# Performance work log

Measured on AMD Instinct MI355X. Metric: run time of the kernel, lower is better.

Reference implementation:

```python
import jax, jax.numpy as jnp
import numpy as np

B, L, D = 4096, 200, 64
N_ITEMS, N_USERS, N_RATINGS = 100000, 100000, 5


def setup_inputs() -> dict:
    key = jax.random.key(0)
    ks = jax.random.split(key, 10)
    nodes = jax.random.randint(ks[0], (B,), 0, N_USERS)
    history_uv = jax.random.randint(ks[1], (B, L), 0, N_ITEMS)
    history_r = jax.random.randint(ks[2], (B, L), 0, N_RATINGS)
    s = 1.0 / np.sqrt(D)
    v2e = jax.random.normal(ks[3], (N_ITEMS, D), dtype=jnp.float32)
    r2e = jax.random.normal(ks[4], (N_RATINGS, D), dtype=jnp.float32)
    # torch Linear: weight is [out, in]
    w1_W = jax.random.uniform(ks[5], (D, 2 * D), dtype=jnp.float32, minval=-s, maxval=s)
    w1_b = jax.random.uniform(ks[6], (D,), dtype=jnp.float32, minval=-s, maxval=s)
    w2_W = jax.random.uniform(ks[7], (D, D), dtype=jnp.float32, minval=-s, maxval=s)
    w2_b = jax.random.uniform(ks[8], (D,), dtype=jnp.float32, minval=-s, maxval=s)
    return {
        "v2e": v2e, "r2e": r2e,
        "w1_W": w1_W, "w1_b": w1_b, "w2_W": w2_W, "w2_b": w2_b,
        "nodes": nodes, "history_uv": history_uv, "history_r": history_r,
    }


def reference(v2e, r2e, w1_W, w1_b, w2_W, w2_b, nodes, history_uv, history_r):
    # Gather item and rating embeddings for every (node, history slot): [B, L, D]
    e_uv = v2e[history_uv]
    e_r = r2e[history_r]
    # concat -> [B, L, 2D], two-layer MLP with ReLU
    x = jnp.concatenate([e_uv, e_r], axis=-1)
    h = jax.nn.relu(jnp.einsum("bli,oi->blo", x, w1_W) + w1_b)
    o = jax.nn.relu(jnp.einsum("bli,oi->blo", h, w2_W) + w2_b)
    # uv=True branch: plain mean over the history dimension (nodes/u2e unused)
    return jnp.mean(o, axis=1)  # [B, D]
```

## Files before the change

kernel.cpp:

```cpp
#include <hip/hip_runtime.h>

#define NITEMS 100000
#define NRATE  5
#define BB     4096
#define LL     200
#define DD     64
#define NBUV   391

typedef short short8  __attribute__((ext_vector_type(8)));
typedef float f32x4   __attribute__((ext_vector_type(4)));
typedef float f32x2   __attribute__((ext_vector_type(2)));
typedef int   i32x4   __attribute__((ext_vector_type(4)));
typedef int   i32x2   __attribute__((ext_vector_type(2)));

static __device__ __forceinline__ short f2bf(float f) {
  return (short)((__builtin_bit_cast(unsigned, f) + 0x8000u) >> 16);
}
static __device__ __forceinline__ unsigned pk2bf(float a, float b) {
  const unsigned ua = __builtin_bit_cast(unsigned, a) + 0x8000u;
  const unsigned ub = __builtin_bit_cast(unsigned, b) + 0x8000u;
  return __builtin_amdgcn_perm(ub, ua, 0x07060302u);
}
static __device__ __forceinline__ int kperm(int p) {
  return ((p & 3) << 4) | (p >> 2);
}

__global__ __launch_bounds__(256) void k_pre(
    const float* __restrict__ v2e, const float* __restrict__ r2e,
    const float* __restrict__ w1W, const float* __restrict__ w1b,
    const float* __restrict__ w2W,
    short* __restrict__ pre_uv, short* __restrict__ w2p,
    float* __restrict__ r5p)
{
  const int tid = threadIdx.x;
  const int blk = blockIdx.x;

  if (blk >= NBUV) {
    for (int idx = tid; idx < 64 * 64; idx += 256) {
      const int o = idx >> 6, p = idx & 63;
      w2p[idx] = f2bf(w2W[o * 64 + kperm(p)]);
    }
    for (int idx = tid; idx < NRATE * 64; idx += 256) {
      const int r = idx >> 6, p = idx & 63;
      const int o = kperm(p);
      const float4* wr = reinterpret_cast<const float4*>(w1W + o * 128 + 64);
      const float4* rr = reinterpret_cast<const float4*>(r2e + r * 64);
      float s = w1b[o];
#pragma unroll
      for (int q = 0; q < 16; ++q) {
        const float4 a = wr[q], b = rr[q];
        s += a.x * b.x + a.y * b.y + a.z * b.z + a.w * b.w;
      }
      r5p[r * 64 + p] = s;
    }
    return;
  }

  const int wave = tid >> 6, lane = tid & 63;
  const int n = lane & 15, quad = lane >> 4;

  short8 bfr[2][4];
#pragma unroll
  for (int nt = 0; nt < 4; ++nt)
#pragma unroll
    for (int kh = 0; kh < 2; ++kh) {
      const float4* p = reinterpret_cast<const float4*>(
          w1W + (nt * 16 + n) * 128 + kh * 32 + quad * 8);
      const float4 x0 = p[0], x1 = p[1];
      i32x4 pk = {(int)pk2bf(x0.x, x0.y), (int)pk2bf(x0.z, x0.w),
                  (int)pk2bf(x1.x, x1.y), (int)pk2bf(x1.z, x1.w)};
      bfr[kh][nt] = __builtin_bit_cast(short8, pk);
    }

  const int ibase_w = blk * 256 + wave * 64;

  float4 cur0, cur1, cur2, cur3;
  {
    const int row = min(ibase_w + n, NITEMS - 1);
    const float4* p = reinterpret_cast<const float4*>(v2e + (size_t)row * 64 + quad * 8);
    cur0 = p[0]; cur1 = p[1];
    const float4* q = reinterpret_cast<const float4*>(v2e + (size_t)row * 64 + 32 + quad * 8);
    cur2 = q[0]; cur3 = q[1];
  }

#pragma unroll
  for (int it = 0; it < 4; ++it) {
    float4 nx0, nx1, nx2, nx3;
    if (it < 3) {
      const int row = min(ibase_w + (it + 1) * 16 + n, NITEMS - 1);
      const float4* p = reinterpret_cast<const float4*>(v2e + (size_t)row * 64 + quad * 8);
      nx0 = p[0]; nx1 = p[1];
      const float4* q = reinterpret_cast<const float4*>(v2e + (size_t)row * 64 + 32 + quad * 8);
      nx2 = q[0]; nx3 = q[1];
    }

    short8 afr[2];
    {
      i32x4 pk0 = {(int)pk2bf(cur0.x, cur0.y), (int)pk2bf(cur0.z, cur0.w),
                   (int)pk2bf(cur1.x, cur1.y), (int)pk2bf(cur1.z, cur1.w)};
      afr[0] = __builtin_bit_cast(short8, pk0);
      i32x4 pk1 = {(int)pk2bf(cur2.x, cur2.y), (int)pk2bf(cur2.z, cur2.w),
                   (int)pk2bf(cur3.x, cur3.y), (int)pk2bf(cur3.z, cur3.w)};
      afr[1] = __builtin_bit_cast(short8, pk1);
    }

    f32x4 d[4];
#pragma unroll
    for (int nt = 0; nt < 4; ++nt) {
      f32x4 z = {0.f, 0.f, 0.f, 0.f};
      z = __builtin_amdgcn_mfma_f32_16x16x32_bf16(afr[0], bfr[0][nt], z, 0, 0, 0);
      z = __builtin_amdgcn_mfma_f32_16x16x32_bf16(afr[1], bfr[1][nt], z, 0, 0, 0);
      d[nt] = z;
    }

#pragma unroll
    for (int r = 0; r < 4; ++r) {
      const int item = ibase_w + it * 16 + quad * 4 + r;
      if (item < NITEMS) {
        i32x2 s = {(int)pk2bf(d[0][r], d[1][r]), (int)pk2bf(d[2][r], d[3][r])};
        *reinterpret_cast<i32x2*>(pre_uv + (size_t)item * 64 + n * 4) = s;
      }
    }

    if (it < 3) { cur0 = nx0; cur1 = nx1; cur2 = nx2; cur3 = nx3; }
  }
}

__global__ __launch_bounds__(256) void k_main(
    const short* __restrict__ pre_uv, const float* __restrict__ r5p,
    const short* __restrict__ w2p, const float* __restrict__ w2b,
    const int* __restrict__ huv, const int* __restrict__ hrr,
    float* __restrict__ out)
{
  __shared__ __align__(16) float s_r5[5 * 68];

  const int tid  = threadIdx.x;
  const int wave = tid >> 6, lane = tid & 63;
  const int n = lane & 15, quad = lane >> 4;
  const int b = blockIdx.x * 4 + wave;

  for (int idx = tid; idx < 5 * 64; idx += 256)
    s_r5[(idx >> 6) * 68 + (idx & 63)] = r5p[idx];

  const int* hu = huv + b * LL;
  const int* hr = hrr + b * LL;

  int iv[13], ir[13];
#pragma unroll
  for (int t = 0; t < 12; ++t) {
    iv[t] = hu[t * 16 + n];
    ir[t] = hr[t * 16 + n];
  }
  {
    const int lc = min(192 + n, LL - 1);
    iv[12] = hu[lc];
    ir[12] = hr[lc];
  }

  short8 u[13][2];
#pragma unroll
  for (int t = 0; t < 13; ++t)
#pragma unroll
    for (int kh = 0; kh < 2; ++kh)
      u[t][kh] = *reinterpret_cast<const short8*>(
          pre_uv + (size_t)iv[t] * 64 + kh * 32 + quad * 8);

  short8 bfr[2][4];
#pragma unroll
  for (int nt = 0; nt < 4; ++nt)
#pragma unroll
    for (int kh = 0; kh < 2; ++kh)
      bfr[kh][nt] = *reinterpret_cast<const short8*>(
          w2p + (nt * 16 + n) * 64 + kh * 32 + quad * 8);

  f32x2 bias2[4];
#pragma unroll
  for (int nt = 0; nt < 4; ++nt) {
    const float bv = w2b[nt * 16 + n];
    bias2[nt] = f32x2{bv, bv};
  }

  __syncthreads();

  const float tailm = (quad < 2) ? 1.0f : 0.0f;
  f32x2 acc2[4] = {{0.f, 0.f}, {0.f, 0.f}, {0.f, 0.f}, {0.f, 0.f}};

#pragma unroll
  for (int t = 0; t < 13; ++t) {
    short8 afr[2];
#pragma unroll
    for (int kh = 0; kh < 2; ++kh) {
      const i32x4 up = __builtin_bit_cast(i32x4, u[t][kh]);
      const f32x2* rp = reinterpret_cast<const f32x2*>(
          s_r5 + ir[t] * 68 + kh * 32 + quad * 8);
      i32x4 hpk;
#pragma unroll
      for (int j = 0; j < 4; ++j) {
        const unsigned p = (unsigned)up[j];
        f32x2 uf = {__builtin_bit_cast(float, p << 16),
                    __builtin_bit_cast(float, p & 0xffff0000u)};
        const f32x2 s = uf + rp[j];
        hpk[j] = (int)pk2bf(fmaxf(s.x, 0.f), fmaxf(s.y, 0.f));
      }
      afr[kh] = __builtin_bit_cast(short8, hpk);
    }

    f32x4 d[4];
#pragma unroll
    for (int nt = 0; nt < 4; ++nt) {
      f32x4 z = {0.f, 0.f, 0.f, 0.f};
      z = __builtin_amdgcn_mfma_f32_16x16x32_bf16(afr[0], bfr[0][nt], z, 0, 0, 0);
      z = __builtin_amdgcn_mfma_f32_16x16x32_bf16(afr[1], bfr[1][nt], z, 0, 0, 0);
      d[nt] = z;
    }

#pragma unroll
    for (int nt = 0; nt < 4; ++nt) {
      f32x2 p0 = f32x2{d[nt][0], d[nt][1]} + bias2[nt];
      f32x2 p1 = f32x2{d[nt][2], d[nt][3]} + bias2[nt];
      p0.x = fmaxf(p0.x, 0.f); p0.y = fmaxf(p0.y, 0.f);
      p1.x = fmaxf(p1.x, 0.f); p1.y = fmaxf(p1.y, 0.f);
      f32x2 s = p0 + p1;
      if (t == 12) { s.x *= tailm; s.y *= tailm; }
      acc2[nt] += s;
    }
  }

  float acc[4];
#pragma unroll
  for (int nt = 0; nt < 4; ++nt) {
    float v = acc2[nt].x + acc2[nt].y;
    v += __shfl_xor(v, 16, 64);
    v += __shfl_xor(v, 32, 64);
    acc[nt] = v;
  }

  out[b * 64 + quad * 16 + n] = acc[quad] * (1.0f / (float)LL);
}

__global__ __launch_bounds__(256) void k_fallback(
    const float* __restrict__ v2e, const float* __restrict__ r2e,
    const float* __restrict__ w1W, const float* __restrict__ w1b,
    const float* __restrict__ w2W, const float* __restrict__ w2b,
    const int* __restrict__ huv, const int* __restrict__ hrr,
    float* __restrict__ out)
{
  __shared__ float sw1[64][129];
  __shared__ float sw2[64][65];
  __shared__ float sx[4][128];
  __shared__ float sh[4][64];
  __shared__ float red[4][64];

  const int tid = threadIdx.x;
  const int wave = tid >> 6, lane = tid & 63;
  const int b = blockIdx.x;

  for (int idx = tid; idx < 64 * 128; idx += 256) sw1[idx >> 7][idx & 127] = w1W[idx];
  for (int idx = tid; idx < 64 * 64; idx += 256) sw2[idx >> 6][idx & 63] = w2W[idx];
  __syncthreads();

  const float b1o = w1b[lane], b2o = w2b[lane];
  float acc = 0.f;

  for (int l = wave; l < LL; l += 4) {
    const int iv = huv[b * LL + l];
    const int ir = hrr[b * LL + l];
    sx[wave][lane]      = v2e[iv * 64 + lane];
    sx[wave][64 + lane] = r2e[ir * 64 + lane];
    __syncthreads();
    float h = b1o;
    for (int i = 0; i < 128; ++i) h += sx[wave][i] * sw1[lane][i];
    sh[wave][lane] = fmaxf(h, 0.f);
    __syncthreads();
    float o = b2o;
    for (int i = 0; i < 64; ++i) o += sh[wave][i] * sw2[lane][i];
    acc += fmaxf(o, 0.f);
  }

  red[wave][lane] = acc;
  __syncthreads();
  if (tid < 64) {
    const float s = red[0][tid] + red[1][tid] + red[2][tid] + red[3][tid];
    out[b * 64 + tid] = s * (1.0f / (float)LL);
  }
}

extern "C" void kernel_launch(void* const* d_in, const int* in_sizes, int n_in,
                              void* d_out, int out_size, void* d_ws, size_t ws_size,
                              hipStream_t stream) {
  (void)in_sizes; (void)n_in; (void)out_size;
  const float* v2e = (const float*)d_in[0];
  const float* r2e = (const float*)d_in[1];
  const float* w1W = (const float*)d_in[2];
  const float* w1b = (const float*)d_in[3];
  const float* w2W = (const float*)d_in[4];
  const float* w2b = (const float*)d_in[5];
  const int* huv = (const int*)d_in[7];
  const int* hrr = (const int*)d_in[8];
  float* out = (float*)d_out;

  const size_t OFF_R5 = (size_t)NITEMS * 64 * sizeof(short);
  const size_t OFF_W2 = OFF_R5 + NRATE * 64 * sizeof(float);
  const size_t NEED   = OFF_W2 + 64 * 64 * sizeof(short);

  if (ws_size >= NEED) {
    short* pre_uv = (short*)d_ws;
    float* r5p    = (float*)((char*)d_ws + OFF_R5);
    short* w2p    = (short*)((char*)d_ws + OFF_W2);

    k_pre<<<NBUV + 1, 256, 0, stream>>>(v2e, r2e, w1W, w1b, w2W, pre_uv, w2p, r5p);
    k_main<<<BB / 4, 256, 0, stream>>>(pre_uv, r5p, w2p, w2b, huv, hrr, out);
  } else {
    k_fallback<<<BB, 256, 0, stream>>>(v2e, r2e, w1W, w1b, w2W, w2b, huv, hrr, out);
  }
}
```

Measured before the change: 115.7 us.

## Grid-stride item tiles in k_pre, per-wave rating table and bias-in-MFMA in k_main

k_pre now launches 512 work blocks, 2048 waves in all, and each wave walks 16-row item tiles with a grid stride of 2048 tiles. The split gives 4 or 3 tiles per wave and drops the bounds clamps, which spreads the v2e projection more evenly over the CUs. k_main gives each wave its own copy of the rating table in LDS, filled by that wave alone, so the block-wide __syncthreads can be removed. It also seeds the MFMA accumulator with the bias, which drops the separate bias adds, and adds a launch bound of 3 blocks per CU that may constrain register allocation.

```diff
diff --git a/kernel.cpp b/kernel.cpp
--- a/kernel.cpp
+++ b/kernel.cpp
@@ -5,7 +5,8 @@
 #define BB     4096
 #define LL     200
 #define DD     64
-#define NBUV   391
+#define NTILES 6250
+#define NWAVES 2048
 
 typedef short short8  __attribute__((ext_vector_type(8)));
 typedef float f32x4   __attribute__((ext_vector_type(4)));
@@ -35,7 +36,7 @@
   const int tid = threadIdx.x;
   const int blk = blockIdx.x;
 
-  if (blk >= NBUV) {
+  if (blk >= 512) {
     for (int idx = tid; idx < 64 * 64; idx += 256) {
       const int o = idx >> 6, p = idx & 63;
       w2p[idx] = f2bf(w2W[o * 64 + kperm(p)]);
@@ -58,6 +59,8 @@
 
   const int wave = tid >> 6, lane = tid & 63;
   const int n = lane & 15, quad = lane >> 4;
+  const int gw = blk * 4 + wave;
+  const int ntile = (gw < (NTILES - 3 * NWAVES)) ? 4 : 3;
 
   short8 bfr[2][4];
 #pragma unroll
@@ -72,25 +75,24 @@
       bfr[kh][nt] = __builtin_bit_cast(short8, pk);
     }
 
-  const int ibase_w = blk * 256 + wave * 64;
-
+  int tile = gw;
   float4 cur0, cur1, cur2, cur3;
   {
-    const int row = min(ibase_w + n, NITEMS - 1);
-    const float4* p = reinterpret_cast<const float4*>(v2e + (size_t)row * 64 + quad * 8);
+    const size_t row = (size_t)(tile * 16 + n);
+    const float4* p = reinterpret_cast<const float4*>(v2e + row * 64 + quad * 8);
     cur0 = p[0]; cur1 = p[1];
-    const float4* q = reinterpret_cast<const float4*>(v2e + (size_t)row * 64 + 32 + quad * 8);
+    const float4* q = reinterpret_cast<const float4*>(v2e + row * 64 + 32 + quad * 8);
     cur2 = q[0]; cur3 = q[1];
   }
 
-#pragma unroll
-  for (int it = 0; it < 4; ++it) {
+  for (int it = 0; it < ntile; ++it) {
+    const int next = tile + NWAVES;
     float4 nx0, nx1, nx2, nx3;
-    if (it < 3) {
-      const int row = min(ibase_w + (it + 1) * 16 + n, NITEMS - 1);
-      const float4* p = reinterpret_cast<const float4*>(v2e + (size_t)row * 64 + quad * 8);
+    if (it + 1 < ntile) {
+      const size_t row = (size_t)(next * 16 + n);
+      const float4* p = reinterpret_cast<const float4*>(v2e + row * 64 + quad * 8);
       nx0 = p[0]; nx1 = p[1];
-      const float4* q = reinterpret_cast<const float4*>(v2e + (size_t)row * 64 + 32 + quad * 8);
+      const float4* q = reinterpret_cast<const float4*>(v2e + row * 64 + 32 + quad * 8);
       nx2 = q[0]; nx3 = q[1];
     }
 
@@ -113,34 +115,37 @@
       d[nt] = z;
     }
 
+    const int ib = tile * 16;
 #pragma unroll
     for (int r = 0; r < 4; ++r) {
-      const int item = ibase_w + it * 16 + quad * 4 + r;
-      if (item < NITEMS) {
-        i32x2 s = {(int)pk2bf(d[0][r], d[1][r]), (int)pk2bf(d[2][r], d[3][r])};
-        *reinterpret_cast<i32x2*>(pre_uv + (size_t)item * 64 + n * 4) = s;
-      }
-    }
-
-    if (it < 3) { cur0 = nx0; cur1 = nx1; cur2 = nx2; cur3 = nx3; }
-  }
-}
-
-__global__ __launch_bounds__(256) void k_main(
+      const int item = ib + quad * 4 + r;
+      i32x2 s = {(int)pk2bf(d[0][r], d[1][r]), (int)pk2bf(d[2][r], d[3][r])};
+      *reinterpret_cast<i32x2*>(pre_uv + (size_t)item * 64 + n * 4) = s;
+    }
+
+    tile = next;
+    cur0 = nx0; cur1 = nx1; cur2 = nx2; cur3 = nx3;
+  }
+}
+
+__global__ __launch_bounds__(256, 3) void k_main(
     const short* __restrict__ pre_uv, const float* __restrict__ r5p,
     const short* __restrict__ w2p, const float* __restrict__ w2b,
     const int* __restrict__ huv, const int* __restrict__ hrr,
     float* __restrict__ out)
 {
-  __shared__ __align__(16) float s_r5[5 * 68];
+  __shared__ __align__(16) float s_r5[4][5 * 68];
 
   const int tid  = threadIdx.x;
   const int wave = tid >> 6, lane = tid & 63;
   const int n = lane & 15, quad = lane >> 4;
   const int b = blockIdx.x * 4 + wave;
 
-  for (int idx = tid; idx < 5 * 64; idx += 256)
-    s_r5[(idx >> 6) * 68 + (idx & 63)] = r5p[idx];
+#pragma unroll
+  for (int i = 0; i < 5; ++i) {
+    const int idx = i * 64 + lane;
+    s_r5[wave][(idx >> 6) * 68 + (idx & 63)] = r5p[idx];
+  }
 
   const int* hu = huv + b * LL;
   const int* hr = hrr + b * LL;
@@ -173,14 +178,12 @@
       bfr[kh][nt] = *reinterpret_cast<const short8*>(
           w2p + (nt * 16 + n) * 64 + kh * 32 + quad * 8);
 
-  f32x2 bias2[4];
+  f32x4 zb[4];
 #pragma unroll
   for (int nt = 0; nt < 4; ++nt) {
     const float bv = w2b[nt * 16 + n];
-    bias2[nt] = f32x2{bv, bv};
-  }
-
-  __syncthreads();
+    zb[nt] = f32x4{bv, bv, bv, bv};
+  }
 
   const float tailm = (quad < 2) ? 1.0f : 0.0f;
   f32x2 acc2[4] = {{0.f, 0.f}, {0.f, 0.f}, {0.f, 0.f}, {0.f, 0.f}};
@@ -192,7 +195,7 @@
     for (int kh = 0; kh < 2; ++kh) {
       const i32x4 up = __builtin_bit_cast(i32x4, u[t][kh]);
       const f32x2* rp = reinterpret_cast<const f32x2*>(
-          s_r5 + ir[t] * 68 + kh * 32 + quad * 8);
+          &s_r5[wave][ir[t] * 68 + kh * 32 + quad * 8]);
       i32x4 hpk;
 #pragma unroll
       for (int j = 0; j < 4; ++j) {
@@ -208,7 +211,7 @@
     f32x4 d[4];
 #pragma unroll
     for (int nt = 0; nt < 4; ++nt) {
-      f32x4 z = {0.f, 0.f, 0.f, 0.f};
+      f32x4 z = zb[nt];
       z = __builtin_amdgcn_mfma_f32_16x16x32_bf16(afr[0], bfr[0][nt], z, 0, 0, 0);
       z = __builtin_amdgcn_mfma_f32_16x16x32_bf16(afr[1], bfr[1][nt], z, 0, 0, 0);
       d[nt] = z;
@@ -216,11 +219,9 @@
 
 #pragma unroll
     for (int nt = 0; nt < 4; ++nt) {
-      f32x2 p0 = f32x2{d[nt][0], d[nt][1]} + bias2[nt];
-      f32x2 p1 = f32x2{d[nt][2], d[nt][3]} + bias2[nt];
-      p0.x = fmaxf(p0.x, 0.f); p0.y = fmaxf(p0.y, 0.f);
-      p1.x = fmaxf(p1.x, 0.f); p1.y = fmaxf(p1.y, 0.f);
-      f32x2 s = p0 + p1;
+      const float m0 = fmaxf(d[nt][0], 0.f), m1 = fmaxf(d[nt][1], 0.f);
+      const float m2 = fmaxf(d[nt][2], 0.f), m3 = fmaxf(d[nt][3], 0.f);
+      f32x2 s = {m0 + m1, m2 + m3};
       if (t == 12) { s.x *= tailm; s.y *= tailm; }
       acc2[nt] += s;
     }
@@ -308,7 +309,7 @@
     float* r5p    = (float*)((char*)d_ws + OFF_R5);
     short* w2p    = (short*)((char*)d_ws + OFF_W2);
 
-    k_pre<<<NBUV + 1, 256, 0, stream>>>(v2e, r2e, w1W, w1b, w2W, pre_uv, w2p, r5p);
+    k_pre<<<513, 256, 0, stream>>>(v2e, r2e, w1W, w1b, w2W, pre_uv, w2p, r5p);
     k_main<<<BB / 4, 256, 0, stream>>>(pre_uv, r5p, w2p, w2b, huv, hrr, out);
   } else {
     k_fallback<<<BB, 256, 0, stream>>>(v2e, r2e, w1W, w1b, w2W, w2b, huv, hrr, out);
```

New measurement: 117.1 us. About the same (+1.2%).
